# Performance work log

Hardware: AMD Instinct MI355X
Metric: run time of the kernel (lower is better)

Reference implementation:

```python
import jax, jax.numpy as jnp
import numpy as np

DIM = 256
NUM_HEADS = 8
B = 4
N = 2048
HEAD_DIM = DIM // NUM_HEADS
SCALE = HEAD_DIM ** -0.5
MASK_NEG = -1000.0  # module uses -1000, not -inf


def _block_mask(n):
    # top-left [n/2, n/2] visible, top-right zeroed; bottom [n/2, n] lower-tri with diagonal offset n/2
    half = n // 2
    top = jnp.concatenate([jnp.ones((half, half)), jnp.zeros((half, half))], axis=1)
    bot = jnp.tril(jnp.ones((half, n)), k=half)
    m = jnp.concatenate([top, bot], axis=0)  # [n, n]
    return jnp.where(m != 0, 0.0, MASK_NEG).astype(jnp.float32)


def setup_inputs() -> dict:
    key = jax.random.key(0)
    k1, k2 = jax.random.split(key, 2)
    x = jax.random.normal(k1, (B, N, DIM), dtype=jnp.float32)
    # fused QKV projection params: Linear(dim, 3*dim, bias=True)
    W_qkv = jax.random.normal(k2, (DIM, 3 * DIM), dtype=jnp.float32) * (DIM ** -0.5)
    b_qkv = jnp.zeros((3 * DIM,), dtype=jnp.float32)
    return {"x": x, "W_qkv": W_qkv, "b_qkv": b_qkv}


def reference(x, W_qkv, b_qkv):
    B_, Nn, C = x.shape
    qkv = x @ W_qkv + b_qkv                                   # [B, N, 3C]
    qkv = qkv.reshape(B_, Nn, 3, NUM_HEADS, C // NUM_HEADS)
    qkv = jnp.transpose(qkv, (2, 0, 3, 1, 4))                 # [3, B, H, N, hd]
    q, k, v = qkv[0] * SCALE, qkv[1], qkv[2]
    attn = jnp.einsum('bhqd,bhkd->bhqk', q, k) + _block_mask(Nn)  # [B, H, N, N]
    attn = jax.nn.softmax(attn, axis=-1)
    out = jnp.einsum('bhqk,bhkd->bhqd', attn, v)              # [B, H, N, hd]
    return jnp.transpose(out, (0, 2, 1, 3)).reshape(B_, Nn, C)
```

## Files before the change

### kernel.cpp

```cpp
#include <hip/hip_runtime.h>
#include <cstdint>
#include <cstddef>

typedef unsigned short u16;
typedef unsigned int u32;
typedef __attribute__((ext_vector_type(8))) __bf16 bf16x8;
typedef __attribute__((ext_vector_type(8))) u16 u16x8;
typedef __attribute__((ext_vector_type(4))) float f32x4;

#define N_SEQ   2048
#define HDIM    32
#define QSCALE_LOG2E 0.2550540261150831f

#if __has_builtin(__builtin_amdgcn_exp2f)
#define EXP2(x) __builtin_amdgcn_exp2f(x)
#else
#define EXP2(x) exp2f(x)
#endif

__device__ __forceinline__ u16 f2bf(float f){
  union { float f; u32 i; } v; v.f = f;
  return (u16)((v.i + 0x7FFFu + ((v.i >> 16) & 1u)) >> 16);
}
__device__ __forceinline__ u32 fbits(float f){
  union { float f; u32 i; } v; v.f = f; return v.i;
}
__device__ __forceinline__ u32 pk2bf(float a, float b){
  return ((fbits(a) + 0x8000u) >> 16) | ((fbits(b) + 0x8000u) & 0xFFFF0000u);
}
__device__ __forceinline__ f32x4 mfma_bf16(bf16x8 a, bf16x8 b, f32x4 c){
  return __builtin_amdgcn_mfma_f32_16x16x32_bf16(a, b, c, 0, 0, 0);
}
union U8 { u16x8 u; bf16x8 b; };
union U2 { u32 w[2]; uint64_t q; };

__global__ __launch_bounds__(256) void wt_kernel(const float* __restrict__ W,
                                                 u16* __restrict__ Wtp){
  int t  = threadIdx.x;
  int tx = t & 31, ty = t >> 5;
  int n0 = blockIdx.x * 32;
  int k0 = blockIdx.y * 32;
#pragma unroll
  for (int i = 0; i < 4; ++i){
    int k = k0 + ty + i*8;
    int c = n0 + tx;
    u16 v = f2bf(W[k*768 + c]);
    Wtp[((c>>4)*8 + (k>>5))*512 + (c&15)*32 + ((k>>3)&3)*8 + (k&7)] = v;
  }
}

__global__ __launch_bounds__(256) void qkv_kernel(const float* __restrict__ X,
                                                  const u16* __restrict__ Wtp,
                                                  const float* __restrict__ bias,
                                                  u16* __restrict__ Q,
                                                  u16* __restrict__ K,
                                                  u16* __restrict__ Vt){
  __shared__ __align__(16) u16 SM[64*264];
  int bid = blockIdx.x;
  int xcd = bid & 7;
  int idx = bid >> 3;
  int mt  = 8*(idx & 15) + xcd;
  int nb  = idx >> 4;
  int tid = threadIdx.x;
  int wave = tid >> 6, lane = tid & 63;
  int l16 = lane & 15, quad = lane >> 4;
  int m0 = mt * 64;
  int n0 = nb * 128;
  const int three = n0 >> 8;

  const float* Xblk = X + m0 * 256;
#pragma unroll
  for (int i = 0; i < 16; ++i){
    int e = i*1024 + tid*4;
    f32x4 v = *(const f32x4*)(Xblk + e);
    int row = e >> 8, col = e & 255;
    U2 pk; pk.w[0] = pk2bf(v[0], v[1]); pk.w[1] = pk2bf(v[2], v[3]);
    *(uint64_t*)(&SM[row*264 + col]) = pk.q;
  }
  __syncthreads();

  int mrow = wave*16 + l16;
  U8 af[8];
#pragma unroll
  for (int k = 0; k < 8; ++k)
    af[k].u = *(const u16x8*)(&SM[mrow*264 + k*32 + quad*8]);
  __syncthreads();

  int b_ = m0 >> 11, nseq0 = m0 & 2047;
  float scl = (three == 0) ? QSCALE_LOG2E : 1.0f;

  for (int jt = 0; jt < 2; ++jt){
    int nn = n0 + jt*64;

    f32x4 acc[4] = {};
#pragma unroll
    for (int k = 0; k < 8; ++k)
#pragma unroll
      for (int s = 0; s < 4; ++s){
        U8 b;
        b.u = *(const u16x8*)(Wtp + (((nn>>4) + s)*8 + k)*512 + l16*32 + quad*8);
        acc[s] = mfma_bf16(af[k].b, b.b, acc[s]);
      }

    if (three == 2){
#pragma unroll
      for (int s = 0; s < 4; ++s){
        int cl = s*16 + l16;
        float bv = bias[nn + cl];
        int tok = wave*16 + quad*4;
        U2 pk;
        pk.w[0] = pk2bf(acc[s][0] + bv, acc[s][1] + bv);
        pk.w[1] = pk2bf(acc[s][2] + bv, acc[s][3] + bv);
        *(uint64_t*)(&SM[cl*68 + tok]) = pk.q;
      }
      __syncthreads();
#pragma unroll
      for (int i = 0; i < 16; ++i){
        int cl = wave*16 + i;
        int c = nn + cl;
        int h = (c >> 5) & 7, d = c & 31;
        int bh = b_*8 + h;
        int kb = (nseq0 >> 5) + (lane >> 5);
        int kk = lane & 31;
        Vt[((bh*64 + kb)*32 + d)*32 + kk] = SM[cl*68 + lane];
      }
    } else {
#pragma unroll
      for (int s = 0; s < 4; ++s){
        int cl = s*16 + l16;
        float bv = bias[nn + cl];
#pragma unroll
        for (int r = 0; r < 4; ++r)
          SM[(wave*16 + quad*4 + r)*68 + cl] = f2bf((acc[s][r] + bv) * scl);
      }
      __syncthreads();
      u16* dst = (three == 0) ? Q : K;
#pragma unroll
      for (int j = 0; j < 2; ++j){
        int unit = tid + j*256;
        int tok = unit & 63;
        int rest = unit >> 6;
        int ph = rest >> 2, chunk = rest & 3;
        int h = ((nn >> 5) + ph) & 7;
        int bh = b_*8 + h;
        u16x8 v = *(const u16x8*)(&SM[tok*68 + ph*32 + chunk*8]);
        *(u16x8*)(&dst[(bh*N_SEQ + nseq0 + tok)*HDIM + chunk*8]) = v;
      }
    }
    __syncthreads();
  }
}

__global__ __launch_bounds__(256, 4) void attn_kernel(const u16* __restrict__ Q,
                                                      const u16* __restrict__ Kg,
                                                      const u16* __restrict__ Vt,
                                                      float* __restrict__ out){
  __shared__ __align__(16) u16 smem[4*2*16*72];
  __shared__ float Lbuf[4][32];
  u16  (*Ps)[2][16][72] = (u16 (*)[2][16][72])smem;
  float (*Obuf)[32][36] = (float (*)[32][36])smem;

  int bid = blockIdx.x;
  int bh = (bid & 7)*4 + ((bid >> 3) & 3);
  int g  = bid >> 5;
  int r0 = g * 64;
  int tid = threadIdx.x, wave = tid >> 6, lane = tid & 63;
  int l16 = lane & 15, quad = lane >> 4;

  const u16* Qb = Q  + bh * (N_SEQ*HDIM);
  const u16* Kb = Kg + bh * (N_SEQ*HDIM);
  const u16* Vb = Vt + bh * (64*32*32);

  const int  T       = (r0 < 1024) ? 16 : (g + 1);
  const bool hasMask = (r0 >= 1024);

  U8 qt[4];
#pragma unroll
  for (int qg = 0; qg < 4; ++qg)
    qt[qg].u = *(const u16x8*)(Qb + (r0 + qg*16 + l16)*HDIM + quad*8);

  U8 onesu;
#pragma unroll
  for (int j = 0; j < 8; ++j) onesu.u[j] = 0x3F80;
  bf16x8 ones = onesu.b;

  f32x4 O[4][2] = {};
  f32x4 L[4] = {};

  for (int t = wave; t < T; t += 4){
    int k0 = t * 64;
    U8 kf[4];
#pragma unroll
    for (int s = 0; s < 4; ++s)
      kf[s].u = *(const u16x8*)(Kb + (k0 + s*16 + l16)*HDIM + quad*8);
    U8 vf[2][2];
#pragma unroll
    for (int kc = 0; kc < 2; ++kc)
#pragma unroll
      for (int nd = 0; nd < 2; ++nd)
        vf[kc][nd].u = *(const u16x8*)(Vb + (size_t)(t*2 + kc)*1024 + (nd*16 + l16)*32 + quad*8);

    bool mask = hasMask && (t == T - 1);

#pragma unroll
    for (int pr = 0; pr < 2; ++pr){
#pragma unroll
      for (int sub = 0; sub < 2; ++sub){
        int qg = pr*2 + sub;
        f32x4 ST[4];
#pragma unroll
        for (int s = 0; s < 4; ++s){
          f32x4 z = {};
          ST[s] = mfma_bf16(kf[s].b, qt[qg].b, z);
        }
        u16 (*P)[72] = Ps[wave][sub];
        if (mask){
          int iq = r0 + qg*16 + l16;
#pragma unroll
          for (int s = 0; s < 4; ++s){
            int jb = k0 + s*16 + quad*4;
            float p0 = (jb+0 > iq) ? 0.0f : EXP2(ST[s][0]);
            float p1 = (jb+1 > iq) ? 0.0f : EXP2(ST[s][1]);
            float p2 = (jb+2 > iq) ? 0.0f : EXP2(ST[s][2]);
            float p3 = (jb+3 > iq) ? 0.0f : EXP2(ST[s][3]);
            U2 pk; pk.w[0] = pk2bf(p0, p1); pk.w[1] = pk2bf(p2, p3);
            *(uint64_t*)(&P[l16][s*16 + quad*4]) = pk.q;
          }
        } else {
#pragma unroll
          for (int s = 0; s < 4; ++s){
            U2 pk;
            pk.w[0] = pk2bf(EXP2(ST[s][0]), EXP2(ST[s][1]));
            pk.w[1] = pk2bf(EXP2(ST[s][2]), EXP2(ST[s][3]));
            *(uint64_t*)(&P[l16][s*16 + quad*4]) = pk.q;
          }
        }
      }

#pragma unroll
      for (int sub = 0; sub < 2; ++sub){
        int qg = pr*2 + sub;
        u16 (*P)[72] = Ps[wave][sub];
#pragma unroll
        for (int kc = 0; kc < 2; ++kc){
          U8 pf; pf.u = *(const u16x8*)(&P[l16][kc*32 + quad*8]);
          O[qg][0] = mfma_bf16(pf.b, vf[kc][0].b, O[qg][0]);
          O[qg][1] = mfma_bf16(pf.b, vf[kc][1].b, O[qg][1]);
          L[qg]    = mfma_bf16(pf.b, ones, L[qg]);
        }
      }
    }
  }

  __syncthreads();

  int b_ = bh >> 3, h = bh & 7;
#pragma unroll
  for (int pass = 0; pass < 2; ++pass){
    if (pass) __syncthreads();
#pragma unroll
    for (int sub = 0; sub < 2; ++sub){
      int qg = pass*2 + sub;
#pragma unroll
      for (int r = 0; r < 4; ++r){
        int row = sub*16 + quad*4 + r;
        Obuf[wave][row][l16]      = O[qg][0][r];
        Obuf[wave][row][16 + l16] = O[qg][1][r];
      }
      if (l16 == 0){
#pragma unroll
        for (int r = 0; r < 4; ++r)
          Lbuf[wave][sub*16 + quad*4 + r] = L[qg][r];
      }
    }
    __syncthreads();
    {
      int row = tid >> 3;
      int c4  = (tid & 7) * 4;
      f32x4 a = *(const f32x4*)(&Obuf[0][row][c4]);
      float Ls = Lbuf[0][row];
#pragma unroll
      for (int w = 1; w < 4; ++w){
        f32x4 b = *(const f32x4*)(&Obuf[w][row][c4]);
        a[0] += b[0]; a[1] += b[1]; a[2] += b[2]; a[3] += b[3];
        Ls += Lbuf[w][row];
      }
      float inv = 1.0f / Ls;
      a[0] *= inv; a[1] *= inv; a[2] *= inv; a[3] *= inv;
      *(f32x4*)(&out[(b_*N_SEQ + r0 + pass*32 + row)*256 + h*32 + c4]) = a;
    }
  }
}

extern "C" void kernel_launch(void* const* d_in, const int* in_sizes, int n_in,
                              void* d_out, int out_size, void* d_ws, size_t ws_size,
                              hipStream_t stream) {
  const float* x    = (const float*)d_in[0];
  const float* W    = (const float*)d_in[1];
  const float* bias = (const float*)d_in[2];
  float* out = (float*)d_out;

  char* ws = (char*)d_ws;
  u16* Wtp   = (u16*)(ws);
  u16* Kbuf  = (u16*)(ws + 393216);
  u16* Vtbuf = (u16*)(ws + 393216 + 4194304);
  u16* Qbuf  = (u16*)(ws + 393216 + 2*4194304);

  wt_kernel  <<<dim3(24, 8), 256, 0, stream>>>(W, Wtp);
  qkv_kernel <<<dim3(768),   256, 0, stream>>>(x, Wtp, bias, Qbuf, Kbuf, Vtbuf);
  attn_kernel<<<dim3(1024),  256, 0, stream>>>(Qbuf, Kbuf, Vtbuf, out);
}
```

Baseline: 123.9 us.

## Halve attention query tile and pass P through ds_bpermute instead of LDS

The attention kernel now handles 32 query rows per block instead of 64 and launches twice as many blocks, giving more parallelism and finer load balance over the causal lower half. The probability tile P is no longer written to and read back from shared memory. Instead it is moved from the MFMA output layout into the A-operand layout with ds_bpermute cross-lane shuffles, which drops the LDS round trip and the P scratch buffer. The cost is that every K/V tile is loaded twice as often across blocks, and there are more bpermute instructions per MFMA.

New measurement: 107.2 us. -13.5%, faster.

```diff
diff --git a/kernel.cpp b/kernel.cpp
--- a/kernel.cpp
+++ b/kernel.cpp
@@ -33,6 +33,7 @@
 }
 union U8 { u16x8 u; bf16x8 b; };
 union U2 { u32 w[2]; uint64_t q; };
+union U4 { u32 w[4]; u16x8 u; bf16x8 b; };
 
 __global__ __launch_bounds__(256) void wt_kernel(const float* __restrict__ W,
                                                  u16* __restrict__ Wtp){
@@ -155,15 +156,13 @@
                                                       const u16* __restrict__ Kg,
                                                       const u16* __restrict__ Vt,
                                                       float* __restrict__ out){
-  __shared__ __align__(16) u16 smem[4*2*16*72];
+  __shared__ __align__(8) float Obuf[4][32][36];
   __shared__ float Lbuf[4][32];
-  u16  (*Ps)[2][16][72] = (u16 (*)[2][16][72])smem;
-  float (*Obuf)[32][36] = (float (*)[32][36])smem;
 
   int bid = blockIdx.x;
   int bh = (bid & 7)*4 + ((bid >> 3) & 3);
   int g  = bid >> 5;
-  int r0 = g * 64;
+  int r0 = g * 32;
   int tid = threadIdx.x, wave = tid >> 6, lane = tid & 63;
   int l16 = lane & 15, quad = lane >> 4;
 
@@ -171,21 +170,24 @@
   const u16* Kb = Kg + bh * (N_SEQ*HDIM);
   const u16* Vb = Vt + bh * (64*32*32);
 
-  const int  T       = (r0 < 1024) ? 16 : (g + 1);
+  const int  T       = (r0 < 1024) ? 16 : (g >> 1) + 1;
   const bool hasMask = (r0 >= 1024);
 
-  U8 qt[4];
-#pragma unroll
-  for (int qg = 0; qg < 4; ++qg)
-    qt[qg].u = *(const u16x8*)(Qb + (r0 + qg*16 + l16)*HDIM + quad*8);
+  U8 qt[2];
+  qt[0].u = *(const u16x8*)(Qb + (r0      + l16)*HDIM + quad*8);
+  qt[1].u = *(const u16x8*)(Qb + (r0 + 16 + l16)*HDIM + quad*8);
 
   U8 onesu;
 #pragma unroll
   for (int j = 0; j < 8; ++j) onesu.u[j] = 0x3F80;
   bf16x8 ones = onesu.b;
 
-  f32x4 O[4][2] = {};
-  f32x4 L[4] = {};
+  f32x4 O[2][2] = {};
+  f32x4 L[2] = {};
+
+  const int la0 = (((quad & 1) * 2) * 16 + l16) * 4;
+  const int la1 = la0 + 64;
+  const bool hiS = (quad >> 1);
 
   for (int t = wave; t < T; t += 4){
     int k0 = t * 64;
@@ -203,92 +205,89 @@
     bool mask = hasMask && (t == T - 1);
 
 #pragma unroll
-    for (int pr = 0; pr < 2; ++pr){
-#pragma unroll
-      for (int sub = 0; sub < 2; ++sub){
-        int qg = pr*2 + sub;
-        f32x4 ST[4];
+    for (int qg = 0; qg < 2; ++qg){
+      f32x4 ST[4];
+#pragma unroll
+      for (int s = 0; s < 4; ++s){
+        f32x4 z = {};
+        ST[s] = mfma_bf16(kf[s].b, qt[qg].b, z);
+      }
+
+      u32 pw[4][2];
+      if (mask){
+        int iq = r0 + qg*16 + l16;
 #pragma unroll
         for (int s = 0; s < 4; ++s){
-          f32x4 z = {};
-          ST[s] = mfma_bf16(kf[s].b, qt[qg].b, z);
+          int jb = k0 + s*16 + quad*4;
+          float p0 = (jb+0 > iq) ? 0.0f : EXP2(ST[s][0]);
+          float p1 = (jb+1 > iq) ? 0.0f : EXP2(ST[s][1]);
+          float p2 = (jb+2 > iq) ? 0.0f : EXP2(ST[s][2]);
+          float p3 = (jb+3 > iq) ? 0.0f : EXP2(ST[s][3]);
+          pw[s][0] = pk2bf(p0, p1); pw[s][1] = pk2bf(p2, p3);
         }
-        u16 (*P)[72] = Ps[wave][sub];
-        if (mask){
-          int iq = r0 + qg*16 + l16;
-#pragma unroll
-          for (int s = 0; s < 4; ++s){
-            int jb = k0 + s*16 + quad*4;
-            float p0 = (jb+0 > iq) ? 0.0f : EXP2(ST[s][0]);
-            float p1 = (jb+1 > iq) ? 0.0f : EXP2(ST[s][1]);
-            float p2 = (jb+2 > iq) ? 0.0f : EXP2(ST[s][2]);
-            float p3 = (jb+3 > iq) ? 0.0f : EXP2(ST[s][3]);
-            U2 pk; pk.w[0] = pk2bf(p0, p1); pk.w[1] = pk2bf(p2, p3);
-            *(uint64_t*)(&P[l16][s*16 + quad*4]) = pk.q;
-          }
-        } else {
-#pragma unroll
-          for (int s = 0; s < 4; ++s){
-            U2 pk;
-            pk.w[0] = pk2bf(EXP2(ST[s][0]), EXP2(ST[s][1]));
-            pk.w[1] = pk2bf(EXP2(ST[s][2]), EXP2(ST[s][3]));
-            *(uint64_t*)(&P[l16][s*16 + quad*4]) = pk.q;
-          }
+      } else {
+#pragma unroll
+        for (int s = 0; s < 4; ++s){
+          pw[s][0] = pk2bf(EXP2(ST[s][0]), EXP2(ST[s][1]));
+          pw[s][1] = pk2bf(EXP2(ST[s][2]), EXP2(ST[s][3]));
         }
       }
 
 #pragma unroll
-      for (int sub = 0; sub < 2; ++sub){
-        int qg = pr*2 + sub;
-        u16 (*P)[72] = Ps[wave][sub];
-#pragma unroll
-        for (int kc = 0; kc < 2; ++kc){
-          U8 pf; pf.u = *(const u16x8*)(&P[l16][kc*32 + quad*8]);
-          O[qg][0] = mfma_bf16(pf.b, vf[kc][0].b, O[qg][0]);
-          O[qg][1] = mfma_bf16(pf.b, vf[kc][1].b, O[qg][1]);
-          L[qg]    = mfma_bf16(pf.b, ones, L[qg]);
-        }
+      for (int kc = 0; kc < 2; ++kc){
+        int s0 = 2*kc, s1 = 2*kc + 1;
+        u32 a00 = __builtin_amdgcn_ds_bpermute(la0, (int)pw[s0][0]);
+        u32 a01 = __builtin_amdgcn_ds_bpermute(la0, (int)pw[s1][0]);
+        u32 a10 = __builtin_amdgcn_ds_bpermute(la0, (int)pw[s0][1]);
+        u32 a11 = __builtin_amdgcn_ds_bpermute(la0, (int)pw[s1][1]);
+        u32 a20 = __builtin_amdgcn_ds_bpermute(la1, (int)pw[s0][0]);
+        u32 a21 = __builtin_amdgcn_ds_bpermute(la1, (int)pw[s1][0]);
+        u32 a30 = __builtin_amdgcn_ds_bpermute(la1, (int)pw[s0][1]);
+        u32 a31 = __builtin_amdgcn_ds_bpermute(la1, (int)pw[s1][1]);
+        U4 A;
+        A.w[0] = hiS ? a01 : a00;
+        A.w[1] = hiS ? a11 : a10;
+        A.w[2] = hiS ? a21 : a20;
+        A.w[3] = hiS ? a31 : a30;
+        O[qg][0] = mfma_bf16(A.b, vf[kc][0].b, O[qg][0]);
+        O[qg][1] = mfma_bf16(A.b, vf[kc][1].b, O[qg][1]);
+        L[qg]    = mfma_bf16(A.b, ones, L[qg]);
       }
     }
   }
 
+#pragma unroll
+  for (int qg = 0; qg < 2; ++qg)
+#pragma unroll
+    for (int r = 0; r < 4; ++r){
+      int row = qg*16 + quad*4 + r;
+      Obuf[wave][row][l16]      = O[qg][0][r];
+      Obuf[wave][row][16 + l16] = O[qg][1][r];
+    }
+  if (l16 == 0){
+#pragma unroll
+    for (int qg = 0; qg < 2; ++qg)
+#pragma unroll
+      for (int r = 0; r < 4; ++r)
+        Lbuf[wave][qg*16 + quad*4 + r] = L[qg][r];
+  }
   __syncthreads();
 
-  int b_ = bh >> 3, h = bh & 7;
-#pragma unroll
-  for (int pass = 0; pass < 2; ++pass){
-    if (pass) __syncthreads();
-#pragma unroll
-    for (int sub = 0; sub < 2; ++sub){
-      int qg = pass*2 + sub;
-#pragma unroll
-      for (int r = 0; r < 4; ++r){
-        int row = sub*16 + quad*4 + r;
-        Obuf[wave][row][l16]      = O[qg][0][r];
-        Obuf[wave][row][16 + l16] = O[qg][1][r];
-      }
-      if (l16 == 0){
-#pragma unroll
-        for (int r = 0; r < 4; ++r)
-          Lbuf[wave][sub*16 + quad*4 + r] = L[qg][r];
-      }
+  {
+    int row = tid >> 3;
+    int c4  = (tid & 7) * 4;
+    f32x4 a = *(const f32x4*)(&Obuf[0][row][c4]);
+    float Ls = Lbuf[0][row];
+#pragma unroll
+    for (int w = 1; w < 4; ++w){
+      f32x4 b = *(const f32x4*)(&Obuf[w][row][c4]);
+      a[0] += b[0]; a[1] += b[1]; a[2] += b[2]; a[3] += b[3];
+      Ls += Lbuf[w][row];
     }
-    __syncthreads();
-    {
-      int row = tid >> 3;
-      int c4  = (tid & 7) * 4;
-      f32x4 a = *(const f32x4*)(&Obuf[0][row][c4]);
-      float Ls = Lbuf[0][row];
-#pragma unroll
-      for (int w = 1; w < 4; ++w){
-        f32x4 b = *(const f32x4*)(&Obuf[w][row][c4]);
-        a[0] += b[0]; a[1] += b[1]; a[2] += b[2]; a[3] += b[3];
-        Ls += Lbuf[w][row];
-      }
-      float inv = 1.0f / Ls;
-      a[0] *= inv; a[1] *= inv; a[2] *= inv; a[3] *= inv;
-      *(f32x4*)(&out[(b_*N_SEQ + r0 + pass*32 + row)*256 + h*32 + c4]) = a;
-    }
+    float inv = 1.0f / Ls;
+    a[0] *= inv; a[1] *= inv; a[2] *= inv; a[3] *= inv;
+    int b_ = bh >> 3, h = bh & 7;
+    *(f32x4*)(&out[(b_*N_SEQ + r0 + row)*256 + h*32 + c4]) = a;
   }
 }
 
@@ -308,5 +307,5 @@
 
   wt_kernel  <<<dim3(24, 8), 256, 0, stream>>>(W, Wtp);
   qkv_kernel <<<dim3(768),   256, 0, stream>>>(x, Wtp, bias, Qbuf, Kbuf, Vtbuf);
-  attn_kernel<<<dim3(1024),  256, 0, stream>>>(Qbuf, Kbuf, Vtbuf, out);
-}
+  attn_kernel<<<dim3(2048),  256, 0, stream>>>(Qbuf, Kbuf, Vtbuf, out);
+}
```
